# Kernel tuning notes

Hardware: AMD Instinct MI355X
Metric: run time of the kernel (lower is better)

The kernel has to match this reference:

```python
import jax, jax.numpy as jnp
import numpy as np

N = 30000          # nodes
E = 480000         # directed edges (avg degree 16)
F_IN = 376         # num_features (hard-coded in module)
HID = 512          # nhid (hard-coded)
NEG_SLOPE = 0.2    # PyG GATConv default negative_slope


def _lin(k, fi, fo):
    return (jax.random.normal(k, (fi, fo), jnp.float32) / np.sqrt(fi)).astype(jnp.float32)


def setup_inputs() -> dict:
    key = jax.random.key(0)
    ks = jax.random.split(key, 16)
    d = {}
    d["x"] = jax.random.normal(ks[0], (N, F_IN), jnp.float32)
    d["edge_index"] = jax.random.randint(ks[1], (2, E), 0, N)
    d["edge_weight"] = jax.random.uniform(ks[2], (E,), jnp.float32)
    # GCNConv(376,512) and GCNConv(512,512)
    d["W1"] = _lin(ks[3], F_IN, HID); d["b1"] = jnp.zeros((HID,), jnp.float32)
    d["W2"] = _lin(ks[4], HID, HID);  d["b2"] = jnp.zeros((HID,), jnp.float32)
    # SAGEConv(512,512): lin_l on aggregated neighbors, lin_r on root
    d["sage_Wl"] = _lin(ks[5], HID, HID)
    d["sage_Wr"] = _lin(ks[6], HID, HID)
    d["sage_b"] = jnp.zeros((HID,), jnp.float32)
    # GATConv(1536, 1, heads=4, concat=False)
    d["gat1_W"] = _lin(ks[7], 3 * HID, 4)
    d["gat1_a_src"] = jax.random.normal(ks[8], (4,), jnp.float32) * 0.1
    d["gat1_a_dst"] = jax.random.normal(ks[9], (4,), jnp.float32) * 0.1
    d["gat1_b"] = jnp.zeros((1,), jnp.float32)
    # GATConv(1536, 1, heads=16, concat=False)
    d["gat2_W"] = _lin(ks[10], 3 * HID, 16)
    d["gat2_a_src"] = jax.random.normal(ks[11], (16,), jnp.float32) * 0.1
    d["gat2_a_dst"] = jax.random.normal(ks[12], (16,), jnp.float32) * 0.1
    d["gat2_b"] = jnp.zeros((1,), jnp.float32)
    return d


def gcn_conv(x, src, dst, ew, W, b, n):
    # PyG GCNConv: add self-loops (weight 1), symmetric normalization
    loop = jnp.arange(n)
    s = jnp.concatenate([src, loop])
    t = jnp.concatenate([dst, loop])
    w = jnp.concatenate([ew, jnp.ones((n,), ew.dtype)])
    deg = jax.ops.segment_sum(w, t, num_segments=n)
    dinv = jnp.where(deg > 0, jax.lax.rsqrt(deg), 0.0)
    norm = dinv[s] * w * dinv[t]                       # [E+N]
    h = x @ W                                           # [N, out]
    out = jax.ops.segment_sum(norm[:, None] * h[s], t, num_segments=n)
    return out + b


def sage_conv(x, src, dst, Wl, Wr, b, n):
    # PyG SAGEConv: mean neighbor aggregation + root transform
    sums = jax.ops.segment_sum(x[src], dst, num_segments=n)
    cnt = jax.ops.segment_sum(jnp.ones((src.shape[0],), x.dtype), dst, num_segments=n)
    mean = sums / jnp.maximum(cnt, 1.0)[:, None]
    return mean @ Wl + x @ Wr + b


def gat_conv(x, src, dst, W, a_src, a_dst, b, n):
    # PyG GATConv (out_channels=1, concat=False -> mean over heads), self-loops added
    loop = jnp.arange(n)
    s = jnp.concatenate([src, loop])
    t = jnp.concatenate([dst, loop])
    h = x @ W                                           # [N, heads] (C=1)
    e = jax.nn.leaky_relu(h[s] * a_src + h[t] * a_dst, NEG_SLOPE)  # [E+N, heads]
    m = jax.ops.segment_max(e, t, num_segments=n)       # stable segment softmax
    ex = jnp.exp(e - m[t])
    den = jax.ops.segment_sum(ex, t, num_segments=n)
    alpha = ex / den[t]
    out = jax.ops.segment_sum(alpha * h[s], t, num_segments=n)     # [N, heads]
    return out.mean(axis=1, keepdims=True) + b          # [N, 1]


def reference(x, edge_index, edge_weight, W1, b1, W2, b2,
              sage_Wl, sage_Wr, sage_b,
              gat1_W, gat1_a_src, gat1_a_dst, gat1_b,
              gat2_W, gat2_a_src, gat2_a_dst, gat2_b):
    n = x.shape[0]
    src, dst = edge_index[0], edge_index[1]
    x1 = jax.nn.relu(gcn_conv(x, src, dst, edge_weight, W1, b1, n))
    x2 = jax.nn.relu(gcn_conv(x1, src, dst, edge_weight, W2, b2, n))
    x3 = jax.nn.relu(sage_conv(x1, src, dst, sage_Wl, sage_Wr, sage_b, n))
    dense_features = jnp.concatenate([x1, x2, x3], axis=1)  # [N, 1536]
    a1 = gat_conv(dense_features, src, dst, gat1_W, gat1_a_src, gat1_a_dst, gat1_b, n)
    a2 = gat_conv(dense_features, src, dst, gat2_W, gat2_a_src, gat2_a_dst, gat2_b, n)
    x_out = jnp.ravel((a1 + a2) * 0.5)                  # [N]
    return x_out, dense_features
```

## Files before the change

kernel.cpp:

```cpp
#include <hip/hip_runtime.h>
#include <hip/hip_bf16.h>
#include <stdint.h>

#define N_NODES 30000
#define M_PAD   30080
#define N_EDGES 480000
#define F_IN 376
#define K1   384
#define HID 512
#define DENSE_F 1536
#define NHEADS 20
#define HG_LD 32

typedef __bf16 bf16_t;
typedef bf16_t bf16x8 __attribute__((ext_vector_type(8)));
typedef float  f32x4  __attribute__((ext_vector_type(4)));

__global__ __launch_bounds__(256) void build_stats(
    const int* __restrict__ dst, const float* __restrict__ ew,
    float* __restrict__ deg, int* __restrict__ cnt)
{
    int e = blockIdx.x * 256 + threadIdx.x;
    if (e >= N_EDGES) return;
    int t = dst[e];
    atomicAdd(&deg[t], ew[e]);
    atomicAdd(&cnt[t], 1);
}

__global__ __launch_bounds__(256) void node_stats(
    float* __restrict__ deg, float* __restrict__ dinv)
{
    int i = blockIdx.x * 256 + threadIdx.x;
    if (i >= N_NODES) return;
    float d = deg[i] + 1.0f;
    deg[i] = d;
    dinv[i] = rsqrtf(d);
}

__global__ __launch_bounds__(1024) void scan_rowptr(
    const int* __restrict__ cnt, int* __restrict__ rowptr, int* __restrict__ woff)
{
    __shared__ int temp[1024];
    __shared__ int carry;
    int t = threadIdx.x;
    if (t == 0) carry = 0;
    __syncthreads();
    for (int base = 0; base < N_NODES; base += 1024) {
        int i = base + t;
        int v = (i < N_NODES) ? cnt[i] : 0;
        temp[t] = v;
        __syncthreads();
        for (int off = 1; off < 1024; off <<= 1) {
            int add = (t >= off) ? temp[t - off] : 0;
            __syncthreads();
            temp[t] += add;
            __syncthreads();
        }
        int excl = temp[t] - v;
        if (i < N_NODES) { rowptr[i] = carry + excl; woff[i] = carry + excl; }
        __syncthreads();
        if (t == 1023) carry += temp[1023];
        __syncthreads();
    }
    if (t == 0) rowptr[N_NODES] = carry;
}

__global__ __launch_bounds__(256) void scatter_csr(
    const int* __restrict__ src, const int* __restrict__ dst,
    const float* __restrict__ ew, int* __restrict__ woff,
    int* __restrict__ col, float* __restrict__ wcsr)
{
    int e = blockIdx.x * 256 + threadIdx.x;
    if (e >= N_EDGES) return;
    int t = dst[e];
    int p = atomicAdd(&woff[t], 1);
    col[p] = src[e];
    wcsr[p] = ew[e];
}

__global__ __launch_bounds__(256) void conv_x(
    const float* __restrict__ x, bf16_t* __restrict__ xb)
{
    int tid = blockIdx.x * 256 + threadIdx.x;
    if (tid >= M_PAD * K1) return;
    int r = tid / K1, c = tid - r * K1;
    float v = (r < N_NODES && c < F_IN) ? x[r * F_IN + c] : 0.f;
    xb[tid] = (bf16_t)v;
}

#define S1 (512 * K1)
#define S2 (512 * 512)
#define S3 (512 * 1024)
#define S4 (128 * DENSE_F)
__global__ __launch_bounds__(256) void pack_weights(
    const float* __restrict__ W1, const float* __restrict__ W2,
    const float* __restrict__ Wl, const float* __restrict__ Wr,
    const float* __restrict__ g1W, const float* __restrict__ g2W,
    const float* __restrict__ a1s, const float* __restrict__ a1d,
    const float* __restrict__ a2s, const float* __restrict__ a2d,
    bf16_t* __restrict__ W1t, bf16_t* __restrict__ W2t,
    bf16_t* __restrict__ Bst, bf16_t* __restrict__ Wgt,
    float* __restrict__ asrc, float* __restrict__ adst)
{
    int tid = blockIdx.x * 256 + threadIdx.x;
    if (tid < S1) {
        int n = tid / K1, k = tid - n * K1;
        W1t[tid] = (bf16_t)((k < F_IN) ? W1[k * HID + n] : 0.f);
    } else if (tid < S1 + S2) {
        int t = tid - S1;
        int n = t >> 9, k = t & 511;
        W2t[t] = (bf16_t)W2[k * HID + n];
    } else if (tid < S1 + S2 + S3) {
        int t = tid - S1 - S2;
        int n = t >> 10, k = t & 1023;
        Bst[t] = (bf16_t)((k < HID) ? Wl[k * HID + n] : Wr[(k - HID) * HID + n]);
    } else if (tid < S1 + S2 + S3 + S4) {
        int t = tid - S1 - S2 - S3;
        int n = t / DENSE_F, k = t - n * DENSE_F;
        float v = (n < 4) ? g1W[k * 4 + n] : (n < NHEADS) ? g2W[k * 16 + (n - 4)] : 0.f;
        Wgt[t] = (bf16_t)v;
    } else if (tid < S1 + S2 + S3 + S4 + NHEADS) {
        int hh = tid - S1 - S2 - S3 - S4;
        asrc[hh] = (hh < 4) ? a1s[hh] : a2s[hh - 4];
        adst[hh] = (hh < 4) ? a1d[hh] : a2d[hh - 4];
    }
}

__global__ __launch_bounds__(256) void gemm_bf16(
    const bf16_t* __restrict__ A1, int lda1, int ksplit,
    const bf16_t* __restrict__ A2, int lda2,
    const bf16_t* __restrict__ Bt, int ldb,
    float* __restrict__ C, bf16_t* __restrict__ Cb, long ldc, int K,
    const float* __restrict__ bias, int ncols)
{
    __shared__ bf16_t As[128 * 32];
    __shared__ bf16_t Bs[128 * 32];
    const int tid = threadIdx.x;
    const int wid = tid >> 6, lane = tid & 63;
    const int li = lane & 15, kq = lane >> 4;
    const int wm = (wid >> 1) * 64, wn = (wid & 1) * 64;
    const long r0 = (long)blockIdx.y * 128;
    const int  n0 = blockIdx.x * 128;

    f32x4 acc[4][4] = {};

    const int s0 = wid * 64 + lane;
    const int s1 = 256 + s0;
    const int am0 = s0 >> 2, ak0 = (s0 & 3) ^ ((am0 >> 1) & 3);
    const int am1 = s1 >> 2, ak1 = (s1 & 3) ^ ((am1 >> 1) & 3);
    const int swz = (li >> 1) & 3;

    for (int k0 = 0; k0 < K; k0 += 32) {
        const bf16_t* Ab; int lda;
        if (k0 < ksplit) { Ab = A1 + k0;            lda = lda1; }
        else             { Ab = A2 + (k0 - ksplit); lda = lda2; }
        __builtin_amdgcn_global_load_lds(
            (const __attribute__((address_space(1))) void*)(Ab + (r0 + am0) * (long)lda + ak0 * 8),
            (__attribute__((address_space(3))) void*)(As + (wid * 64) * 8), 16, 0, 0);
        __builtin_amdgcn_global_load_lds(
            (const __attribute__((address_space(1))) void*)(Ab + (r0 + am1) * (long)lda + ak1 * 8),
            (__attribute__((address_space(3))) void*)(As + (256 + wid * 64) * 8), 16, 0, 0);
        __builtin_amdgcn_global_load_lds(
            (const __attribute__((address_space(1))) void*)(Bt + (n0 + am0) * (long)ldb + k0 + ak0 * 8),
            (__attribute__((address_space(3))) void*)(Bs + (wid * 64) * 8), 16, 0, 0);
        __builtin_amdgcn_global_load_lds(
            (const __attribute__((address_space(1))) void*)(Bt + (n0 + am1) * (long)ldb + k0 + ak1 * 8),
            (__attribute__((address_space(3))) void*)(Bs + (256 + wid * 64) * 8), 16, 0, 0);
        __syncthreads();

        bf16x8 a[4], b[4];
#pragma unroll
        for (int f = 0; f < 4; ++f) {
            int m = wm + f * 16 + li;
            a[f] = *(const bf16x8*)(As + m * 32 + ((kq ^ swz) * 8));
            int n = wn + f * 16 + li;
            b[f] = *(const bf16x8*)(Bs + n * 32 + ((kq ^ swz) * 8));
        }
#pragma unroll
        for (int fm = 0; fm < 4; ++fm)
#pragma unroll
            for (int fn = 0; fn < 4; ++fn)
                acc[fm][fn] = __builtin_amdgcn_mfma_f32_16x16x32_bf16(
                    a[fm], b[fn], acc[fm][fn], 0, 0, 0);
        __syncthreads();
    }

#pragma unroll
    for (int fm = 0; fm < 4; ++fm) {
#pragma unroll
        for (int r = 0; r < 4; ++r) {
            long row = r0 + wm + fm * 16 + kq * 4 + r;
            if (row >= N_NODES) continue;
#pragma unroll
            for (int fn = 0; fn < 4; ++fn) {
                int colg = n0 + wn + fn * 16 + li;
                if (colg >= ncols) continue;
                float v = acc[fm][fn][r];
                if (bias) v = fmaxf(v + bias[colg], 0.f);
                if (C)  C[row * ldc + colg]  = v;
                if (Cb) Cb[row * ldc + colg] = (bf16_t)v;
            }
        }
    }
}

__global__ __launch_bounds__(64) void agg_x(
    const bf16_t* __restrict__ xb, const int* __restrict__ rowptr,
    const int* __restrict__ col, const float* __restrict__ wcsr,
    const float* __restrict__ dinv, const float* __restrict__ deg,
    bf16_t* __restrict__ aggx)
{
    int i = blockIdx.x;
    int c = threadIdx.x * 8;
    bool act = (c < K1);
    float di = dinv[i];
    float selfw = 1.0f / deg[i];
    float acc0[8] = {}, acc1[8] = {};
    if (act) {
        bf16x8 sv = *(const bf16x8*)(xb + (long)i * K1 + c);
#pragma unroll
        for (int j = 0; j < 8; ++j) acc0[j] = selfw * (float)sv[j];
    }
    int e = rowptr[i], e1 = rowptr[i + 1];
    for (; e + 1 < e1; e += 2) {
        int sA = col[e], sB = col[e + 1];
        float wA = dinv[sA] * wcsr[e] * di;
        float wB = dinv[sB] * wcsr[e + 1] * di;
        if (act) {
            bf16x8 vA = *(const bf16x8*)(xb + (long)sA * K1 + c);
            bf16x8 vB = *(const bf16x8*)(xb + (long)sB * K1 + c);
#pragma unroll
            for (int j = 0; j < 8; ++j) {
                acc0[j] = fmaf(wA, (float)vA[j], acc0[j]);
                acc1[j] = fmaf(wB, (float)vB[j], acc1[j]);
            }
        }
    }
    if (e < e1) {
        int sA = col[e];
        float wA = dinv[sA] * wcsr[e] * di;
        if (act) {
            bf16x8 vA = *(const bf16x8*)(xb + (long)sA * K1 + c);
#pragma unroll
            for (int j = 0; j < 8; ++j) acc0[j] = fmaf(wA, (float)vA[j], acc0[j]);
        }
    }
    if (act) {
        bf16x8 ob;
#pragma unroll
        for (int j = 0; j < 8; ++j) ob[j] = (bf16_t)(acc0[j] + acc1[j]);
        *reinterpret_cast<bf16x8*>(aggx + (long)i * K1 + c) = ob;
    }
}

__global__ __launch_bounds__(64) void agg_x1(
    const bf16_t* __restrict__ x1b ,
    const int* __restrict__ rowptr, const int* __restrict__ col,
    const float* __restrict__ wcsr, const float* __restrict__ dinv,
    const float* __restrict__ deg, const int* __restrict__ cnt,
    bf16_t* __restrict__ gbf, bf16_t* __restrict__ meanb)
{
    int i = blockIdx.x;
    int c = threadIdx.x * 8;
    float di = dinv[i];
    float selfw = 1.0f / deg[i];
    bf16x8 sv = *(const bf16x8*)(x1b + (long)i * DENSE_F + c);
    float g0[8], g1[8], m0[8], m1[8];
#pragma unroll
    for (int j = 0; j < 8; ++j) {
        g0[j] = selfw * (float)sv[j];
        g1[j] = 0.f; m0[j] = 0.f; m1[j] = 0.f;
    }
    int e = rowptr[i], e1 = rowptr[i + 1];
    for (; e + 1 < e1; e += 2) {
        int sA = col[e], sB = col[e + 1];
        float wA = dinv[sA] * wcsr[e] * di;
        float wB = dinv[sB] * wcsr[e + 1] * di;
        bf16x8 vA = *(const bf16x8*)(x1b + (long)sA * DENSE_F + c);
        bf16x8 vB = *(const bf16x8*)(x1b + (long)sB * DENSE_F + c);
#pragma unroll
        for (int j = 0; j < 8; ++j) {
            float fA = (float)vA[j], fB = (float)vB[j];
            g0[j] = fmaf(wA, fA, g0[j]);
            g1[j] = fmaf(wB, fB, g1[j]);
            m0[j] += fA;
            m1[j] += fB;
        }
    }
    if (e < e1) {
        int sA = col[e];
        float wA = dinv[sA] * wcsr[e] * di;
        bf16x8 vA = *(const bf16x8*)(x1b + (long)sA * DENSE_F + c);
#pragma unroll
        for (int j = 0; j < 8; ++j) {
            float fA = (float)vA[j];
            g0[j] = fmaf(wA, fA, g0[j]);
            m0[j] += fA;
        }
    }
    float inv = 1.0f / fmaxf((float)cnt[i], 1.0f);
    bf16x8 og, om;
#pragma unroll
    for (int j = 0; j < 8; ++j) {
        og[j] = (bf16_t)(g0[j] + g1[j]);
        om[j] = (bf16_t)((m0[j] + m1[j]) * inv);
    }
    *reinterpret_cast<bf16x8*>(gbf   + (long)i * HID + c) = og;
    *reinterpret_cast<bf16x8*>(meanb + (long)i * HID + c) = om;
}

__global__ __launch_bounds__(64) void gat_agg(
    const float* __restrict__ hgat, const int* __restrict__ rowptr,
    const int* __restrict__ col, const float* __restrict__ asrc,
    const float* __restrict__ adst, const float* __restrict__ b1p,
    const float* __restrict__ b2p, float* __restrict__ xout)
{
    int i = blockIdx.x;
    int lane = threadIdx.x;
    int h = (lane < NHEADS) ? lane : 0;
    float hg_i = hgat[(long)i * HG_LD + h];
    float as = asrc[h], ad = adst[h];
    float adhg = ad * hg_i;
    float ev = hg_i * as + adhg;
    ev = ev > 0.f ? ev : 0.2f * ev;
    float ex = __expf(ev);
    float den0 = ex, og0 = ex * hg_i, den1 = 0.f, og1 = 0.f;
    int e = rowptr[i], e1 = rowptr[i + 1];
    for (; e + 1 < e1; e += 2) {
        int sA = col[e], sB = col[e + 1];
        float hA = hgat[(long)sA * HG_LD + h];
        float hB = hgat[(long)sB * HG_LD + h];
        float tA = fmaf(hA, as, adhg); tA = tA > 0.f ? tA : 0.2f * tA;
        float tB = fmaf(hB, as, adhg); tB = tB > 0.f ? tB : 0.2f * tB;
        float xA = __expf(tA), xB = __expf(tB);
        den0 += xA; og0 = fmaf(xA, hA, og0);
        den1 += xB; og1 = fmaf(xB, hB, og1);
    }
    if (e < e1) {
        int sA = col[e];
        float hA = hgat[(long)sA * HG_LD + h];
        float tA = fmaf(hA, as, adhg); tA = tA > 0.f ? tA : 0.2f * tA;
        float xA = __expf(tA);
        den0 += xA; og0 = fmaf(xA, hA, og0);
    }
    float out = (lane < NHEADS) ? (og0 + og1) / (den0 + den1) : 0.f;
    float s4 = out + __shfl_xor(out, 1);
    s4 += __shfl_xor(s4, 2);
    float g0 = __shfl(s4, 0);
    float g1 = __shfl(s4, 4);
    float g2 = __shfl(s4, 8);
    float g3 = __shfl(s4, 12);
    float g4 = __shfl(s4, 16);
    if (lane == 0) {
        float a1 = g0 * 0.25f + b1p[0];
        float a2 = (g1 + g2 + g3 + g4) * 0.0625f + b2p[0];
        xout[i] = 0.5f * (a1 + a2);
    }
}

extern "C" void kernel_launch(void* const* d_in, const int* in_sizes, int n_in,
                              void* d_out, int out_size, void* d_ws, size_t ws_size,
                              hipStream_t stream) {
    (void)in_sizes; (void)n_in; (void)out_size; (void)ws_size;
    const float* x    = (const float*)d_in[0];
    const int*   ei   = (const int*)d_in[1];
    const float* ew   = (const float*)d_in[2];
    const float* W1   = (const float*)d_in[3];
    const float* b1   = (const float*)d_in[4];
    const float* W2   = (const float*)d_in[5];
    const float* b2   = (const float*)d_in[6];
    const float* sWl  = (const float*)d_in[7];
    const float* sWr  = (const float*)d_in[8];
    const float* sb   = (const float*)d_in[9];
    const float* g1W  = (const float*)d_in[10];
    const float* g1as = (const float*)d_in[11];
    const float* g1ad = (const float*)d_in[12];
    const float* g1b  = (const float*)d_in[13];
    const float* g2W  = (const float*)d_in[14];
    const float* g2as = (const float*)d_in[15];
    const float* g2ad = (const float*)d_in[16];
    const float* g2b  = (const float*)d_in[17];

    const int* src = ei;
    const int* dst = ei + N_EDGES;

    float* xout  = (float*)d_out;
    float* dense = xout + N_NODES;

    size_t off = 0;
    auto alloc = [&](size_t nbytes) -> void* {
        void* p = (char*)d_ws + off;
        off += (nbytes + 255) & ~(size_t)255;
        return p;
    };
    bf16_t* dense_bf = (bf16_t*)alloc((size_t)M_PAD * DENSE_F * 2);
    bf16_t* x_bf     = (bf16_t*)alloc((size_t)M_PAD * K1 * 2);
    bf16_t* aggx_bf  = (bf16_t*)alloc((size_t)M_PAD * K1 * 2);
    bf16_t* g_bf     = (bf16_t*)alloc((size_t)M_PAD * HID * 2);
    bf16_t* mean_bf  = (bf16_t*)alloc((size_t)M_PAD * HID * 2);
    float*  hgat     = (float*)alloc((size_t)M_PAD * HG_LD * 4);
    bf16_t* W1t      = (bf16_t*)alloc((size_t)512 * K1 * 2);
    bf16_t* W2t      = (bf16_t*)alloc((size_t)512 * 512 * 2);
    bf16_t* Bst      = (bf16_t*)alloc((size_t)512 * 1024 * 2);
    bf16_t* Wgt      = (bf16_t*)alloc((size_t)128 * DENSE_F * 2);
    float*  deg      = (float*)alloc((size_t)N_NODES * 4);
    float*  dinv     = (float*)alloc((size_t)N_NODES * 4);
    float*  asrc     = (float*)alloc(32 * 4);
    float*  adst     = (float*)alloc(32 * 4);
    int*    cnt      = (int*)alloc((size_t)N_NODES * 4);
    int*    rowp     = (int*)alloc((size_t)(N_NODES + 1) * 4);
    int*    woff     = (int*)alloc((size_t)N_NODES * 4);
    int*    colx     = (int*)alloc((size_t)N_EDGES * 4);
    float*  wcsr     = (float*)alloc((size_t)N_EDGES * 4);

    const int EB = (N_EDGES + 255) / 256;
    const int NB = (N_NODES + 255) / 256;

    hipMemsetAsync(deg, 0, (size_t)N_NODES * 4, stream);
    hipMemsetAsync(cnt, 0, (size_t)N_NODES * 4, stream);
    build_stats<<<EB, 256, 0, stream>>>(dst, ew, deg, cnt);
    node_stats<<<NB, 256, 0, stream>>>(deg, dinv);
    scan_rowptr<<<1, 1024, 0, stream>>>(cnt, rowp, woff);
    scatter_csr<<<EB, 256, 0, stream>>>(src, dst, ew, woff, colx, wcsr);

    conv_x<<<(M_PAD * K1 + 255) / 256, 256, 0, stream>>>(x, x_bf);
    pack_weights<<<(S1 + S2 + S3 + S4 + NHEADS + 255) / 256, 256, 0, stream>>>(
        W1, W2, sWl, sWr, g1W, g2W, g1as, g1ad, g2as, g2ad,
        W1t, W2t, Bst, Wgt, asrc, adst);

    const dim3 gB(256);
    const dim3 g512(HID / 128, M_PAD / 128);
    const dim3 g128(1, M_PAD / 128);

    agg_x<<<N_NODES, 64, 0, stream>>>(x_bf, rowp, colx, wcsr, dinv, deg, aggx_bf);
    gemm_bf16<<<g512, gB, 0, stream>>>(aggx_bf, K1, K1, aggx_bf, K1, W1t, K1,
                                       dense, dense_bf, DENSE_F, K1, b1, 512);

    agg_x1<<<N_NODES, 64, 0, stream>>>(dense_bf, rowp, colx, wcsr, dinv, deg, cnt,
                                       g_bf, mean_bf);
    gemm_bf16<<<g512, gB, 0, stream>>>(g_bf, HID, HID, g_bf, HID, W2t, HID,
                                       dense + HID, dense_bf + HID, DENSE_F,
                                       HID, b2, 512);
    gemm_bf16<<<g512, gB, 0, stream>>>(mean_bf, HID, HID, dense_bf, DENSE_F,
                                       Bst, 1024, dense + 2 * HID,
                                       dense_bf + 2 * HID, DENSE_F, 1024, sb, 512);

    gemm_bf16<<<g128, gB, 0, stream>>>(dense_bf, DENSE_F, DENSE_F, dense_bf, DENSE_F,
                                       Wgt, DENSE_F, hgat, nullptr, HG_LD,
                                       DENSE_F, nullptr, HG_LD);
    gat_agg<<<N_NODES, 64, 0, stream>>>(hgat, rowp, colx, asrc, adst, g1b, g2b, xout);
}
```

Measured before the change: 799.9 us.

## Fuse prologue kernels, warp-shuffle scan, 4-node blocks, split-K GAT projection

Merges the edge-stats, x conversion and weight-packing kernels into one prologue launch, and replaces the single-block Hillis-Steele rowptr scan with a per-thread serial plus warp-shuffle scan that also computes deg and dinv. The three per-node aggregation kernels now handle four nodes per 256-thread block instead of one node per 64-thread block. The narrow GAT projection GEMM is split over K into two z-slices that combine through atomicAdd into a zeroed hgat buffer. The aim is fewer launches, a shorter serial scan and better occupancy, at the cost of an extra memset, float atomics with order-dependent summation, and more registers in the scan.

```diff
diff --git a/kernel.cpp b/kernel.cpp
--- a/kernel.cpp
+++ b/kernel.cpp
@@ -16,83 +16,21 @@
 typedef bf16_t bf16x8 __attribute__((ext_vector_type(8)));
 typedef float  f32x4  __attribute__((ext_vector_type(4)));
 
-__global__ __launch_bounds__(256) void build_stats(
-    const int* __restrict__ dst, const float* __restrict__ ew,
-    float* __restrict__ deg, int* __restrict__ cnt)
-{
-    int e = blockIdx.x * 256 + threadIdx.x;
-    if (e >= N_EDGES) return;
-    int t = dst[e];
-    atomicAdd(&deg[t], ew[e]);
-    atomicAdd(&cnt[t], 1);
-}
-
-__global__ __launch_bounds__(256) void node_stats(
-    float* __restrict__ deg, float* __restrict__ dinv)
-{
-    int i = blockIdx.x * 256 + threadIdx.x;
-    if (i >= N_NODES) return;
-    float d = deg[i] + 1.0f;
-    deg[i] = d;
-    dinv[i] = rsqrtf(d);
-}
-
-__global__ __launch_bounds__(1024) void scan_rowptr(
-    const int* __restrict__ cnt, int* __restrict__ rowptr, int* __restrict__ woff)
-{
-    __shared__ int temp[1024];
-    __shared__ int carry;
-    int t = threadIdx.x;
-    if (t == 0) carry = 0;
-    __syncthreads();
-    for (int base = 0; base < N_NODES; base += 1024) {
-        int i = base + t;
-        int v = (i < N_NODES) ? cnt[i] : 0;
-        temp[t] = v;
-        __syncthreads();
-        for (int off = 1; off < 1024; off <<= 1) {
-            int add = (t >= off) ? temp[t - off] : 0;
-            __syncthreads();
-            temp[t] += add;
-            __syncthreads();
-        }
-        int excl = temp[t] - v;
-        if (i < N_NODES) { rowptr[i] = carry + excl; woff[i] = carry + excl; }
-        __syncthreads();
-        if (t == 1023) carry += temp[1023];
-        __syncthreads();
-    }
-    if (t == 0) rowptr[N_NODES] = carry;
-}
-
-__global__ __launch_bounds__(256) void scatter_csr(
-    const int* __restrict__ src, const int* __restrict__ dst,
-    const float* __restrict__ ew, int* __restrict__ woff,
-    int* __restrict__ col, float* __restrict__ wcsr)
-{
-    int e = blockIdx.x * 256 + threadIdx.x;
-    if (e >= N_EDGES) return;
-    int t = dst[e];
-    int p = atomicAdd(&woff[t], 1);
-    col[p] = src[e];
-    wcsr[p] = ew[e];
-}
-
-__global__ __launch_bounds__(256) void conv_x(
-    const float* __restrict__ x, bf16_t* __restrict__ xb)
-{
-    int tid = blockIdx.x * 256 + threadIdx.x;
-    if (tid >= M_PAD * K1) return;
-    int r = tid / K1, c = tid - r * K1;
-    float v = (r < N_NODES && c < F_IN) ? x[r * F_IN + c] : 0.f;
-    xb[tid] = (bf16_t)v;
-}
-
 #define S1 (512 * K1)
 #define S2 (512 * 512)
 #define S3 (512 * 1024)
 #define S4 (128 * DENSE_F)
-__global__ __launch_bounds__(256) void pack_weights(
+#define PW_ELEMS (S1 + S2 + S3 + S4 + NHEADS)
+
+#define EB_BLOCKS ((N_EDGES + 255) / 256)
+#define CX_BLOCKS ((M_PAD * K1) / 256)
+#define PW_BLOCKS ((PW_ELEMS + 255) / 256)
+#define PRO_BLOCKS (EB_BLOCKS + CX_BLOCKS + PW_BLOCKS)
+
+__global__ __launch_bounds__(256) void prologue(
+    const int* __restrict__ dst, const float* __restrict__ ew,
+    float* __restrict__ deg, int* __restrict__ cnt,
+    const float* __restrict__ x, bf16_t* __restrict__ xb,
     const float* __restrict__ W1, const float* __restrict__ W2,
     const float* __restrict__ Wl, const float* __restrict__ Wr,
     const float* __restrict__ g1W, const float* __restrict__ g2W,
@@ -102,28 +40,108 @@
     bf16_t* __restrict__ Bst, bf16_t* __restrict__ Wgt,
     float* __restrict__ asrc, float* __restrict__ adst)
 {
-    int tid = blockIdx.x * 256 + threadIdx.x;
-    if (tid < S1) {
-        int n = tid / K1, k = tid - n * K1;
-        W1t[tid] = (bf16_t)((k < F_IN) ? W1[k * HID + n] : 0.f);
-    } else if (tid < S1 + S2) {
-        int t = tid - S1;
-        int n = t >> 9, k = t & 511;
-        W2t[t] = (bf16_t)W2[k * HID + n];
-    } else if (tid < S1 + S2 + S3) {
-        int t = tid - S1 - S2;
-        int n = t >> 10, k = t & 1023;
-        Bst[t] = (bf16_t)((k < HID) ? Wl[k * HID + n] : Wr[(k - HID) * HID + n]);
-    } else if (tid < S1 + S2 + S3 + S4) {
-        int t = tid - S1 - S2 - S3;
-        int n = t / DENSE_F, k = t - n * DENSE_F;
-        float v = (n < 4) ? g1W[k * 4 + n] : (n < NHEADS) ? g2W[k * 16 + (n - 4)] : 0.f;
-        Wgt[t] = (bf16_t)v;
-    } else if (tid < S1 + S2 + S3 + S4 + NHEADS) {
-        int hh = tid - S1 - S2 - S3 - S4;
-        asrc[hh] = (hh < 4) ? a1s[hh] : a2s[hh - 4];
-        adst[hh] = (hh < 4) ? a1d[hh] : a2d[hh - 4];
-    }
+    int b = blockIdx.x;
+    if (b < EB_BLOCKS) {
+        int e = b * 256 + threadIdx.x;
+        if (e >= N_EDGES) return;
+        int t = dst[e];
+        atomicAdd(&deg[t], ew[e]);
+        atomicAdd(&cnt[t], 1);
+    } else if (b < EB_BLOCKS + CX_BLOCKS) {
+        int tid = (b - EB_BLOCKS) * 256 + threadIdx.x;
+        int r = tid / K1, c = tid - r * K1;
+        float v = (r < N_NODES && c < F_IN) ? x[r * F_IN + c] : 0.f;
+        xb[tid] = (bf16_t)v;
+    } else {
+        int tid = (b - EB_BLOCKS - CX_BLOCKS) * 256 + threadIdx.x;
+        if (tid < S1) {
+            int n = tid / K1, k = tid - n * K1;
+            W1t[tid] = (bf16_t)((k < F_IN) ? W1[k * HID + n] : 0.f);
+        } else if (tid < S1 + S2) {
+            int t = tid - S1;
+            int n = t >> 9, k = t & 511;
+            W2t[t] = (bf16_t)W2[k * HID + n];
+        } else if (tid < S1 + S2 + S3) {
+            int t = tid - S1 - S2;
+            int n = t >> 10, k = t & 1023;
+            Bst[t] = (bf16_t)((k < HID) ? Wl[k * HID + n] : Wr[(k - HID) * HID + n]);
+        } else if (tid < S1 + S2 + S3 + S4) {
+            int t = tid - S1 - S2 - S3;
+            int n = t / DENSE_F, k = t - n * DENSE_F;
+            float v = (n < 4) ? g1W[k * 4 + n] : (n < NHEADS) ? g2W[k * 16 + (n - 4)] : 0.f;
+            Wgt[t] = (bf16_t)v;
+        } else if (tid < S1 + S2 + S3 + S4 + NHEADS) {
+            int hh = tid - S1 - S2 - S3 - S4;
+            asrc[hh] = (hh < 4) ? a1s[hh] : a2s[hh - 4];
+            adst[hh] = (hh < 4) ? a1d[hh] : a2d[hh - 4];
+        }
+    }
+}
+
+#define SEG 30
+__global__ __launch_bounds__(1024) void scan_rowptr_fast(
+    const int* __restrict__ cnt, int* __restrict__ rowptr, int* __restrict__ woff,
+    float* __restrict__ deg, float* __restrict__ dinv)
+{
+    int t = threadIdx.x;
+    int base = t * SEG;
+    int v[SEG];
+    int sum = 0;
+#pragma unroll
+    for (int j = 0; j < SEG; ++j) {
+        int i = base + j;
+        int c = (i < N_NODES) ? cnt[i] : 0;
+        v[j] = c;
+        sum += c;
+        if (i < N_NODES) {
+            float d = deg[i] + 1.0f;
+            deg[i] = d;
+            dinv[i] = rsqrtf(d);
+        }
+    }
+    int lane = t & 63;
+    int wid = t >> 6;
+    int s = sum;
+#pragma unroll
+    for (int off = 1; off < 64; off <<= 1) {
+        int u = __shfl_up(s, off);
+        if (lane >= off) s += u;
+    }
+    __shared__ int wsum[16];
+    if (lane == 63) wsum[wid] = s;
+    __syncthreads();
+    if (t < 16) {
+        int ws = wsum[t];
+#pragma unroll
+        for (int off = 1; off < 16; off <<= 1) {
+            int u = __shfl_up(ws, off);
+            if (t >= off) ws += u;
+        }
+        wsum[t] = ws;
+    }
+    __syncthreads();
+    int carry = (wid > 0) ? wsum[wid - 1] : 0;
+    int excl = carry + s - sum;
+#pragma unroll
+    for (int j = 0; j < SEG; ++j) {
+        int i = base + j;
+        if (i < N_NODES) { rowptr[i] = excl; woff[i] = excl; }
+        excl += v[j];
+    }
+    if (t == 1023) rowptr[N_NODES] = excl;
+}
+
+__global__ __launch_bounds__(256) void scatter_csr(
+    const int* __restrict__ src, const int* __restrict__ dst,
+    const float* __restrict__ ew, int* __restrict__ woff,
+    int* __restrict__ col, float* __restrict__ wcsr)
+{
+    int e = blockIdx.x * 256 + threadIdx.x;
+    if (e >= N_EDGES) return;
+    int t = dst[e];
+    int p = atomicAdd(&woff[t], 1);
+    col[p] = src[e];
+    wcsr[p] = ew[e];
 }
 
 __global__ __launch_bounds__(256) void gemm_bf16(
@@ -131,7 +149,7 @@
     const bf16_t* __restrict__ A2, int lda2,
     const bf16_t* __restrict__ Bt, int ldb,
     float* __restrict__ C, bf16_t* __restrict__ Cb, long ldc, int K,
-    const float* __restrict__ bias, int ncols)
+    const float* __restrict__ bias, int ncols, int accum)
 {
     __shared__ bf16_t As[128 * 32];
     __shared__ bf16_t Bs[128 * 32];
@@ -142,6 +160,10 @@
     const long r0 = (long)blockIdx.y * 128;
     const int  n0 = blockIdx.x * 128;
 
+    const int kb = K / (int)gridDim.z;
+    const int k_lo = (int)blockIdx.z * kb;
+    const int k_hi = k_lo + kb;
+
     f32x4 acc[4][4] = {};
 
     const int s0 = wid * 64 + lane;
@@ -150,7 +172,7 @@
     const int am1 = s1 >> 2, ak1 = (s1 & 3) ^ ((am1 >> 1) & 3);
     const int swz = (li >> 1) & 3;
 
-    for (int k0 = 0; k0 < K; k0 += 32) {
+    for (int k0 = k_lo; k0 < k_hi; k0 += 32) {
         const bf16_t* Ab; int lda;
         if (k0 < ksplit) { Ab = A1 + k0;            lda = lda1; }
         else             { Ab = A2 + (k0 - ksplit); lda = lda2; }
@@ -197,21 +219,25 @@
                 if (colg >= ncols) continue;
                 float v = acc[fm][fn][r];
                 if (bias) v = fmaxf(v + bias[colg], 0.f);
-                if (C)  C[row * ldc + colg]  = v;
+                if (C) {
+                    if (accum) atomicAdd(&C[row * ldc + colg], v);
+                    else       C[row * ldc + colg] = v;
+                }
                 if (Cb) Cb[row * ldc + colg] = (bf16_t)v;
             }
         }
     }
 }
 
-__global__ __launch_bounds__(64) void agg_x(
+__global__ __launch_bounds__(256) void agg_x(
     const bf16_t* __restrict__ xb, const int* __restrict__ rowptr,
     const int* __restrict__ col, const float* __restrict__ wcsr,
     const float* __restrict__ dinv, const float* __restrict__ deg,
     bf16_t* __restrict__ aggx)
 {
-    int i = blockIdx.x;
-    int c = threadIdx.x * 8;
+    int i = blockIdx.x * 4 + (threadIdx.x >> 6);
+    int lane = threadIdx.x & 63;
+    int c = lane * 8;
     bool act = (c < K1);
     float di = dinv[i];
     float selfw = 1.0f / deg[i];
@@ -253,15 +279,16 @@
     }
 }
 
-__global__ __launch_bounds__(64) void agg_x1(
+__global__ __launch_bounds__(256) void agg_x1(
     const bf16_t* __restrict__ x1b ,
     const int* __restrict__ rowptr, const int* __restrict__ col,
     const float* __restrict__ wcsr, const float* __restrict__ dinv,
     const float* __restrict__ deg, const int* __restrict__ cnt,
     bf16_t* __restrict__ gbf, bf16_t* __restrict__ meanb)
 {
-    int i = blockIdx.x;
-    int c = threadIdx.x * 8;
+    int i = blockIdx.x * 4 + (threadIdx.x >> 6);
+    int lane = threadIdx.x & 63;
+    int c = lane * 8;
     float di = dinv[i];
     float selfw = 1.0f / deg[i];
     bf16x8 sv = *(const bf16x8*)(x1b + (long)i * DENSE_F + c);
@@ -309,14 +336,14 @@
     *reinterpret_cast<bf16x8*>(meanb + (long)i * HID + c) = om;
 }
 
-__global__ __launch_bounds__(64) void gat_agg(
+__global__ __launch_bounds__(256) void gat_agg(
     const float* __restrict__ hgat, const int* __restrict__ rowptr,
     const int* __restrict__ col, const float* __restrict__ asrc,
     const float* __restrict__ adst, const float* __restrict__ b1p,
     const float* __restrict__ b2p, float* __restrict__ xout)
 {
-    int i = blockIdx.x;
-    int lane = threadIdx.x;
+    int i = blockIdx.x * 4 + (threadIdx.x >> 6);
+    int lane = threadIdx.x & 63;
     int h = (lane < NHEADS) ? lane : 0;
     float hg_i = hgat[(long)i * HG_LD + h];
     float as = asrc[h], ad = adst[h];
@@ -413,40 +440,38 @@
     int*    colx     = (int*)alloc((size_t)N_EDGES * 4);
     float*  wcsr     = (float*)alloc((size_t)N_EDGES * 4);
 
-    const int EB = (N_EDGES + 255) / 256;
-    const int NB = (N_NODES + 255) / 256;
+    const int EB = EB_BLOCKS;
 
     hipMemsetAsync(deg, 0, (size_t)N_NODES * 4, stream);
     hipMemsetAsync(cnt, 0, (size_t)N_NODES * 4, stream);
-    build_stats<<<EB, 256, 0, stream>>>(dst, ew, deg, cnt);
-    node_stats<<<NB, 256, 0, stream>>>(deg, dinv);
-    scan_rowptr<<<1, 1024, 0, stream>>>(cnt, rowp, woff);
-    scatter_csr<<<EB, 256, 0, stream>>>(src, dst, ew, woff, colx, wcsr);
-
-    conv_x<<<(M_PAD * K1 + 255) / 256, 256, 0, stream>>>(x, x_bf);
-    pack_weights<<<(S1 + S2 + S3 + S4 + NHEADS + 255) / 256, 256, 0, stream>>>(
+    hipMemsetAsync(hgat, 0, (size_t)M_PAD * HG_LD * 4, stream);
+
+    prologue<<<PRO_BLOCKS, 256, 0, stream>>>(
+        dst, ew, deg, cnt, x, x_bf,
         W1, W2, sWl, sWr, g1W, g2W, g1as, g1ad, g2as, g2ad,
         W1t, W2t, Bst, Wgt, asrc, adst);
+    scan_rowptr_fast<<<1, 1024, 0, stream>>>(cnt, rowp, woff, deg, dinv);
+    scatter_csr<<<EB, 256, 0, stream>>>(src, dst, ew, woff, colx, wcsr);
 
     const dim3 gB(256);
     const dim3 g512(HID / 128, M_PAD / 128);
-    const dim3 g128(1, M_PAD / 128);
-
-    agg_x<<<N_NODES, 64, 0, stream>>>(x_bf, rowp, colx, wcsr, dinv, deg, aggx_bf);
+    const dim3 g128z(1, M_PAD / 128, 2);
+
+    agg_x<<<N_NODES / 4, 256, 0, stream>>>(x_bf, rowp, colx, wcsr, dinv, deg, aggx_bf);
     gemm_bf16<<<g512, gB, 0, stream>>>(aggx_bf, K1, K1, aggx_bf, K1, W1t, K1,
-                                       dense, dense_bf, DENSE_F, K1, b1, 512);
-
-    agg_x1<<<N_NODES, 64, 0, stream>>>(dense_bf, rowp, colx, wcsr, dinv, deg, cnt,
-                                       g_bf, mean_bf);
+                                       dense, dense_bf, DENSE_F, K1, b1, 512, 0);
+
+    agg_x1<<<N_NODES / 4, 256, 0, stream>>>(dense_bf, rowp, colx, wcsr, dinv, deg, cnt,
+                                            g_bf, mean_bf);
     gemm_bf16<<<g512, gB, 0, stream>>>(g_bf, HID, HID, g_bf, HID, W2t, HID,
                                        dense + HID, dense_bf + HID, DENSE_F,
-                                       HID, b2, 512);
+                                       HID, b2, 512, 0);
     gemm_bf16<<<g512, gB, 0, stream>>>(mean_bf, HID, HID, dense_bf, DENSE_F,
                                        Bst, 1024, dense + 2 * HID,
-                                       dense_bf + 2 * HID, DENSE_F, 1024, sb, 512);
-
-    gemm_bf16<<<g128, gB, 0, stream>>>(dense_bf, DENSE_F, DENSE_F, dense_bf, DENSE_F,
-                                       Wgt, DENSE_F, hgat, nullptr, HG_LD,
-                                       DENSE_F, nullptr, HG_LD);
-    gat_agg<<<N_NODES, 64, 0, stream>>>(hgat, rowp, colx, asrc, adst, g1b, g2b, xout);
-}
+                                       dense_bf + 2 * HID, DENSE_F, 1024, sb, 512, 0);
+
+    gemm_bf16<<<g128z, gB, 0, stream>>>(dense_bf, DENSE_F, DENSE_F, dense_bf, DENSE_F,
+                                        Wgt, DENSE_F, hgat, nullptr, HG_LD,
+                                        DENSE_F, nullptr, HG_LD, 1);
+    gat_agg<<<N_NODES / 4, 256, 0, stream>>>(hgat, rowp, colx, asrc, adst, g1b, g2b, xout);
+}
```

New measurement: 837.7 us. 4.7% more time.
